# Kernel optimization log

Measured on AMD Instinct MI355X. Metric: run time of the kernel, lower is better.

## Reference

```python
import jax, jax.numpy as jnp
import numpy as np

B, T, C = 8, 1024, 2048
N_HEAD = 16
HEAD = C // N_HEAD  # 128


def setup_inputs() -> dict:
    key = jax.random.key(0)
    k1, k2, k3 = jax.random.split(key, 3)
    scale = 0.02
    x = jax.random.normal(k1, (B, T, C), dtype=jnp.float32)
    W_attn = jax.random.normal(k2, (C, 3 * C), dtype=jnp.float32) * scale
    b_attn = jnp.zeros((3 * C,), dtype=jnp.float32)
    W_proj = jax.random.normal(k3, (C, C), dtype=jnp.float32) * scale
    b_proj = jnp.zeros((C,), dtype=jnp.float32)
    return {"x": x, "W_attn": W_attn, "b_attn": b_attn, "W_proj": W_proj, "b_proj": b_proj}


def reference(x, W_attn, b_attn, W_proj, b_proj):
    Bq, Tq, Cq = x.shape
    qkv = x @ W_attn + b_attn                       # [B,T,3C]
    q, k, v = jnp.split(qkv, 3, axis=2)             # each [B,T,C]
    def heads(t):
        return t.reshape(Bq, Tq, N_HEAD, HEAD).transpose(0, 2, 1, 3)  # [B,H,T,D]
    q, k, v = heads(q), heads(k), heads(v)
    scores = jnp.einsum('bhqd,bhkd->bhqk', q, k) / jnp.sqrt(jnp.float32(HEAD))
    causal = jnp.tril(jnp.ones((Tq, Tq), dtype=bool))
    scores = jnp.where(causal, scores, jnp.float32(-1e9))
    attn = jax.nn.softmax(scores, axis=-1)          # [B,H,T,T]
    y = jnp.einsum('bhqk,bhkd->bhqd', attn, v)      # [B,H,T,D]
    y = y.transpose(0, 2, 1, 3).reshape(Bq, Tq, Cq) # [B,T,C]
    return y @ W_proj + b_proj
```

## Files before the change

### kernel.cpp

```cpp
#include <hip/hip_runtime.h>
#include <hip/hip_bf16.h>


typedef unsigned short u16;
typedef unsigned int u32;
typedef __bf16 bf16x8 __attribute__((ext_vector_type(8)));
typedef float f32x4 __attribute__((ext_vector_type(4)));

#define B_ 8
#define T_ 1024
#define C_ 2048
#define NH 16
#define HD 128
#define BH (B_*NH)

__device__ __forceinline__ u16 f2b(float f){
  __bf16 h = (__bf16)f; return __builtin_bit_cast(u16, h);
}
__device__ __forceinline__ unsigned pk2(float x, float y){
  return (unsigned)f2b(x) | ((unsigned)f2b(y) << 16);
}
__device__ __forceinline__ bf16x8 ldfrag(const u16* p){
  uint4 u = *(const uint4*)p; return __builtin_bit_cast(bf16x8, u);
}
__device__ __forceinline__ void glds16(const u16* g, const u16* l){
  __builtin_amdgcn_global_load_lds(
      (const __attribute__((address_space(1))) void*)g,
      (__attribute__((address_space(3))) void*)l, 16, 0, 0);
}
__device__ __forceinline__ void sbar(){
  __builtin_amdgcn_sched_barrier(0);
  __builtin_amdgcn_s_barrier();
  __builtin_amdgcn_sched_barrier(0);
}

__global__ __launch_bounds__(256) void prep(
    const float* __restrict__ W_attn, u16* __restrict__ Wat,
    const float* __restrict__ W_proj, u16* __restrict__ Wpt,
    const float4* __restrict__ x4, ushort4* __restrict__ xb4, int do_cvt)
{
  __shared__ u16 tile[64][65];
  const int t = threadIdx.x;
  const int z = blockIdx.z;
  if (z == 1 && blockIdx.x >= 32){
    if (!do_cvt) return;
    const int n4 = (B_*T_*C_)/4;
    int i = ((blockIdx.x - 32)*32 + blockIdx.y)*256 + t;
    const int stride = 2048*256;
    for (; i < n4; i += stride){
      float4 f = x4[i];
      ushort4 o; o.x = f2b(f.x); o.y = f2b(f.y); o.z = f2b(f.z); o.w = f2b(f.w);
      xb4[i] = o;
    }
    return;
  }
  const float* in = (z == 0) ? W_attn : W_proj;
  u16* outp       = (z == 0) ? Wat    : Wpt;
  const int R = 2048, C = (z == 0) ? 6144 : 2048;
  const int r0 = blockIdx.y * 64, c0 = blockIdx.x * 64;
#pragma unroll
  for (int ii = 0; ii < 16; ++ii){
    int idx = t + ii*256; int r = idx >> 6, c = idx & 63;
    tile[r][c] = f2b(in[(size_t)(r0 + r)*C + c0 + c]);
  }
  __syncthreads();
#pragma unroll
  for (int ii = 0; ii < 16; ++ii){
    int idx = t + ii*256; int r = idx >> 6, c = idx & 63;
    outp[(size_t)(c0 + r)*R + r0 + c] = tile[c][r];
  }
}

__device__ __forceinline__ void qkv_epilogue(
    const f32x4 acc[4][4], const float* bias, int bx, int by,
    int wm, int wn, int lq, int ln,
    u16* qb, u16* kb, u16* vb)
{
  const int tensor = bx >> 4, h = bx & 15, b = by >> 3, t0 = (by & 7)*128;
  u16* tb = tensor==0 ? qb : (tensor==1 ? kb : vb);
  u16* op = tb + ((size_t)(b*NH + h)*T_ + t0)*HD;
#pragma unroll
  for (int j=0;j<4;j++){
    const float bv = bias[bx*128 + wn*64 + j*16 + ln];
    const int n = wn*64 + j*16 + ln;
#pragma unroll
    for (int i=0;i<4;i++){
      const int m0 = wm*64 + i*16 + lq*4;
#pragma unroll
      for (int r=0;r<4;r++)
        op[(size_t)(m0 + r)*HD + n] = f2b(acc[i][j][r] + bv);
    }
  }
}

__global__ __launch_bounds__(512,2) void gemm_qkv_8p(
    const u16* __restrict__ Xb, const u16* __restrict__ Wt,
    const float* __restrict__ bias,
    u16* __restrict__ qb, u16* __restrict__ kb, u16* __restrict__ vb)
{
  __shared__ u16 lds[2][2][256*64];
  const int t = threadIdx.x;
  const int lane = t & 63, wid = t >> 6;
  const int lq = lane >> 4, ln = lane & 15;
  const int wm = wid >> 2, wn = wid & 3;

  const int bid0 = blockIdx.x;
  const int bid = (bid0 & 7)*96 + (bid0 >> 3);
  const int bx = bid % 24, by = bid / 24;

  const int rl  = (wid << 4) + (lane >> 3);
  const int sw0 = (lane & 7) ^ (rl & 7);
  const u16* Ag = Xb + ((size_t)(by*256) + rl)*2048;
  const u16* Bg = Wt + ((size_t)(bx*256) + rl)*2048;
  const size_t q0off = (size_t)sw0*8;
  const size_t q1off = (size_t)8*2048 + (size_t)sw0*8;

#define STAGE(buf_, op_, h_, T_) do { \
    const u16* s_ = (op_ ? Bg : Ag) + (size_t)(h_)*(128*2048) + (size_t)(T_)*64; \
    const u16* d_ = &lds[buf_][op_][(((h_)*128) + (wid<<4))*64]; \
    glds16(s_ + q0off, d_); \
    glds16(s_ + q1off, d_ + 8*64); \
  } while(0)

  const int swr0 = (0*4 + lq) ^ (ln & 7);
  const int swr1 = (1*4 + lq) ^ (ln & 7);

  const f32x4 fz = {0.f,0.f,0.f,0.f};
  f32x4 acc[8][4];
#pragma unroll
  for (int f=0;f<8;f++)
#pragma unroll
    for (int g=0;g<4;g++) acc[f][g] = fz;

  STAGE(0,0,0,0); STAGE(0,0,1,0); STAGE(0,1,0,0); STAGE(0,1,1,0);
  STAGE(1,1,0,1); STAGE(1,1,1,1); STAGE(1,0,0,1);
  asm volatile("s_waitcnt vmcnt(6)" ::: "memory");
  sbar();

  for (int T = 0; T < 32; ++T){
    const int b = T & 1;
    const u16* As = lds[b][0];
    const u16* Bs = lds[b][1];
    bf16x8 a0[4][2], a4[4][2], bfr[4][2];

#pragma unroll
    for (int f=0;f<4;f++){
      a0[f][0]  = ldfrag(&As[(wm*128 + f*16 + ln)*64 + swr0*8]);
      a0[f][1]  = ldfrag(&As[(wm*128 + f*16 + ln)*64 + swr1*8]);
      bfr[f][0] = ldfrag(&Bs[(wn*64  + f*16 + ln)*64 + swr0*8]);
      bfr[f][1] = ldfrag(&Bs[(wn*64  + f*16 + ln)*64 + swr1*8]);
    }
    if (T+1 < 32) STAGE(b^1, 0, 1, T+1);
    sbar();
    __builtin_amdgcn_s_setprio(1);
#pragma unroll
    for (int f=0;f<4;f++)
#pragma unroll
      for (int g=0;g<2;g++){
        acc[f][g] = __builtin_amdgcn_mfma_f32_16x16x32_bf16(a0[f][0], bfr[g][0], acc[f][g], 0,0,0);
        acc[f][g] = __builtin_amdgcn_mfma_f32_16x16x32_bf16(a0[f][1], bfr[g][1], acc[f][g], 0,0,0);
      }
    __builtin_amdgcn_s_setprio(0);
    sbar();

#pragma unroll
    for (int f=0;f<4;f++){
      a4[f][0] = ldfrag(&As[(wm*128 + (f+4)*16 + ln)*64 + swr0*8]);
      a4[f][1] = ldfrag(&As[(wm*128 + (f+4)*16 + ln)*64 + swr1*8]);
    }
    if (T+2 < 32) STAGE(b, 1, 0, T+2);
    sbar();
    __builtin_amdgcn_s_setprio(1);
#pragma unroll
    for (int f=0;f<4;f++)
#pragma unroll
      for (int g=0;g<2;g++){
        acc[f+4][g] = __builtin_amdgcn_mfma_f32_16x16x32_bf16(a4[f][0], bfr[g][0], acc[f+4][g], 0,0,0);
        acc[f+4][g] = __builtin_amdgcn_mfma_f32_16x16x32_bf16(a4[f][1], bfr[g][1], acc[f+4][g], 0,0,0);
      }
    __builtin_amdgcn_s_setprio(0);
    sbar();

    if (T+2 < 32) STAGE(b, 1, 1, T+2);
    sbar();
    __builtin_amdgcn_s_setprio(1);
#pragma unroll
    for (int f=0;f<4;f++)
#pragma unroll
      for (int g=2;g<4;g++){
        acc[f+4][g] = __builtin_amdgcn_mfma_f32_16x16x32_bf16(a4[f][0], bfr[g][0], acc[f+4][g], 0,0,0);
        acc[f+4][g] = __builtin_amdgcn_mfma_f32_16x16x32_bf16(a4[f][1], bfr[g][1], acc[f+4][g], 0,0,0);
      }
    __builtin_amdgcn_s_setprio(0);
    sbar();

    if (T+2 < 32) STAGE(b, 0, 0, T+2);
    if (T >= 30) asm volatile("s_waitcnt vmcnt(0)" ::: "memory");
    else         asm volatile("s_waitcnt vmcnt(6)" ::: "memory");
    sbar();
    __builtin_amdgcn_s_setprio(1);
#pragma unroll
    for (int f=0;f<4;f++)
#pragma unroll
      for (int g=2;g<4;g++){
        acc[f][g] = __builtin_amdgcn_mfma_f32_16x16x32_bf16(a0[f][0], bfr[g][0], acc[f][g], 0,0,0);
        acc[f][g] = __builtin_amdgcn_mfma_f32_16x16x32_bf16(a0[f][1], bfr[g][1], acc[f][g], 0,0,0);
      }
    __builtin_amdgcn_s_setprio(0);
    sbar();
  }
#undef STAGE

  const int tensor = bx >> 3;
  u16* tb = tensor==0 ? qb : (tensor==1 ? kb : vb);
  const int m_base = by*256 + wm*128;
#pragma unroll
  for (int g=0; g<4; ++g){
    const int ncol = (bx & 7)*256 + wn*64 + g*16 + ln;
    const float bv = bias[tensor*2048 + ncol];
    const int h = ncol >> 7, d = ncol & 127;
#pragma unroll
    for (int f=0; f<8; ++f){
      const int m0 = m_base + f*16 + lq*4;
      const int bb = m0 >> 10, tt = m0 & 1023;
      u16* op = tb + ((size_t)(bb*NH + h)*T_ + tt)*HD + d;
#pragma unroll
      for (int r=0;r<4;++r)
        op[(size_t)r*HD] = f2b(acc[f][g][r] + bv);
    }
  }
}

__global__ __launch_bounds__(512,2) void gemm_proj_8p(
    const u16* __restrict__ Y, const u16* __restrict__ Wt,
    const float* __restrict__ bias, float* __restrict__ outp)
{
  __shared__ u16 lds[2][2][256*64];
  const int t = threadIdx.x;
  const int lane = t & 63, wid = t >> 6;
  const int lq = lane >> 4, ln = lane & 15;
  const int wm = wid >> 2, wn = wid & 3;

  const int bid0 = blockIdx.x;
  const int bid = (bid0 & 7)*32 + (bid0 >> 3);
  const int bx = bid & 7, by = bid >> 3;

  const int rl  = (wid << 4) + (lane >> 3);
  const int sw0 = (lane & 7) ^ (rl & 7);
  const u16* Bg = Wt + ((size_t)(bx*256) + rl)*2048;
  const size_t bq0 = (size_t)sw0*8;
  const size_t arow0 = ((size_t)(by >> 2)*16)*1024 + (size_t)(by & 3)*256 + rl;

#define STAGEP(buf_, op_, h_, Tt_) do { \
    const u16* d_ = &lds[buf_][op_][(((h_)*128) + (wid<<4))*64]; \
    if (op_){ \
      const u16* s_ = Bg + (size_t)(h_)*(128*2048) + (size_t)(Tt_)*64; \
      glds16(s_ + bq0, d_); \
      glds16(s_ + (size_t)8*2048 + bq0, d_ + 8*64); \
    } else { \
      const u16* s_ = Y + (arow0 + (size_t)((Tt_) >> 1)*1024 + (size_t)(h_)*128)*128 \
                        + ((Tt_) & 1)*64 + sw0*8; \
      glds16(s_, d_); \
      glds16(s_ + 8*128, d_ + 8*64); \
    } \
  } while(0)

  const int swr0 = (0*4 + lq) ^ (ln & 7);
  const int swr1 = (1*4 + lq) ^ (ln & 7);

  const f32x4 fz = {0.f,0.f,0.f,0.f};
  f32x4 acc[8][4];
#pragma unroll
  for (int f=0;f<8;f++)
#pragma unroll
    for (int g=0;g<4;g++) acc[f][g] = fz;

  STAGEP(0,0,0,0); STAGEP(0,0,1,0); STAGEP(0,1,0,0); STAGEP(0,1,1,0);
  STAGEP(1,1,0,1); STAGEP(1,1,1,1); STAGEP(1,0,0,1);
  asm volatile("s_waitcnt vmcnt(6)" ::: "memory");
  sbar();

  for (int T = 0; T < 32; ++T){
    const int b = T & 1;
    const u16* As = lds[b][0];
    const u16* Bs = lds[b][1];
    bf16x8 a0[4][2], a4[4][2], bfr[4][2];

#pragma unroll
    for (int f=0;f<4;f++){
      a0[f][0]  = ldfrag(&As[(wm*128 + f*16 + ln)*64 + swr0*8]);
      a0[f][1]  = ldfrag(&As[(wm*128 + f*16 + ln)*64 + swr1*8]);
      bfr[f][0] = ldfrag(&Bs[(wn*64  + f*16 + ln)*64 + swr0*8]);
      bfr[f][1] = ldfrag(&Bs[(wn*64  + f*16 + ln)*64 + swr1*8]);
    }
    if (T+1 < 32) STAGEP(b^1, 0, 1, T+1);
    sbar();
    __builtin_amdgcn_s_setprio(1);
#pragma unroll
    for (int f=0;f<4;f++)
#pragma unroll
      for (int g=0;g<2;g++){
        acc[f][g] = __builtin_amdgcn_mfma_f32_16x16x32_bf16(a0[f][0], bfr[g][0], acc[f][g], 0,0,0);
        acc[f][g] = __builtin_amdgcn_mfma_f32_16x16x32_bf16(a0[f][1], bfr[g][1], acc[f][g], 0,0,0);
      }
    __builtin_amdgcn_s_setprio(0);
    sbar();

#pragma unroll
    for (int f=0;f<4;f++){
      a4[f][0] = ldfrag(&As[(wm*128 + (f+4)*16 + ln)*64 + swr0*8]);
      a4[f][1] = ldfrag(&As[(wm*128 + (f+4)*16 + ln)*64 + swr1*8]);
    }
    if (T+2 < 32) STAGEP(b, 1, 0, T+2);
    sbar();
    __builtin_amdgcn_s_setprio(1);
#pragma unroll
    for (int f=0;f<4;f++)
#pragma unroll
      for (int g=0;g<2;g++){
        acc[f+4][g] = __builtin_amdgcn_mfma_f32_16x16x32_bf16(a4[f][0], bfr[g][0], acc[f+4][g], 0,0,0);
        acc[f+4][g] = __builtin_amdgcn_mfma_f32_16x16x32_bf16(a4[f][1], bfr[g][1], acc[f+4][g], 0,0,0);
      }
    __builtin_amdgcn_s_setprio(0);
    sbar();

    if (T+2 < 32) STAGEP(b, 1, 1, T+2);
    sbar();
    __builtin_amdgcn_s_setprio(1);
#pragma unroll
    for (int f=0;f<4;f++)
#pragma unroll
      for (int g=2;g<4;g++){
        acc[f+4][g] = __builtin_amdgcn_mfma_f32_16x16x32_bf16(a4[f][0], bfr[g][0], acc[f+4][g], 0,0,0);
        acc[f+4][g] = __builtin_amdgcn_mfma_f32_16x16x32_bf16(a4[f][1], bfr[g][1], acc[f+4][g], 0,0,0);
      }
    __builtin_amdgcn_s_setprio(0);
    sbar();

    if (T+2 < 32) STAGEP(b, 0, 0, T+2);
    if (T >= 30) asm volatile("s_waitcnt vmcnt(0)" ::: "memory");
    else         asm volatile("s_waitcnt vmcnt(6)" ::: "memory");
    sbar();
    __builtin_amdgcn_s_setprio(1);
#pragma unroll
    for (int f=0;f<4;f++)
#pragma unroll
      for (int g=2;g<4;g++){
        acc[f][g] = __builtin_amdgcn_mfma_f32_16x16x32_bf16(a0[f][0], bfr[g][0], acc[f][g], 0,0,0);
        acc[f][g] = __builtin_amdgcn_mfma_f32_16x16x32_bf16(a0[f][1], bfr[g][1], acc[f][g], 0,0,0);
      }
    __builtin_amdgcn_s_setprio(0);
    sbar();
  }
#undef STAGEP

  const int m_base = by*256 + wm*128;
#pragma unroll
  for (int g=0; g<4; ++g){
    const int ncol = bx*256 + wn*64 + g*16 + ln;
    const float bv = bias[ncol];
#pragma unroll
    for (int f=0; f<8; ++f){
      const int m0 = m_base + f*16 + lq*4;
      float* op = outp + (size_t)m0*2048 + ncol;
#pragma unroll
      for (int r=0;r<4;++r)
        op[(size_t)r*2048] = acc[f][g][r] + bv;
    }
  }
}

__global__ __launch_bounds__(256,2) void gemm_qkv_f32(
    const float* __restrict__ X, const u16* __restrict__ Wt, const float* __restrict__ bias,
    u16* __restrict__ qb, u16* __restrict__ kb, u16* __restrict__ vb)
{
  __shared__ u16 As[128*32];
  __shared__ u16 Bs[128*32];
  const int t = threadIdx.x;
  const int bx = blockIdx.x, by = blockIdx.y;
  const int lane = t & 63, wv = t >> 6;
  const int lq = lane >> 4, ln = lane & 15;
  const int wm = wv >> 1, wn = wv & 1;

  const int ar = t >> 1, ah = t & 1;
  const float* Ap = X + (size_t)(by*128 + ar)*2048 + ah*16;
  u16* AsW = &As[ar*32 + ah*16];

  const int c0 = t, c1 = 256 + t;
  const u16* Bp0 = Wt + (size_t)(bx*128 + (c0 >> 2))*2048 + (c0 & 3)*8;
  const u16* Bp1 = Wt + (size_t)(bx*128 + (c1 >> 2))*2048 + (c1 & 3)*8;
  const u16* BsW0 = &Bs[(wv*64)*8];
  const u16* BsW1 = &Bs[(256 + wv*64)*8];

  const f32x4 fz = {0.f,0.f,0.f,0.f};
  f32x4 acc[4][4];
#pragma unroll
  for (int i=0;i<4;i++)
#pragma unroll
    for (int j=0;j<4;j++) acc[i][j] = fz;

  for (int kt = 0; kt < 64; ++kt){
    float4 a0 = *(const float4*)(Ap);
    float4 a1 = *(const float4*)(Ap + 4);
    float4 a2 = *(const float4*)(Ap + 8);
    float4 a3 = *(const float4*)(Ap + 12);
    Ap += 32;
    __syncthreads();
    uint4 w0, w1;
    w0.x = pk2(a0.x,a0.y); w0.y = pk2(a0.z,a0.w);
    w0.z = pk2(a1.x,a1.y); w0.w = pk2(a1.z,a1.w);
    w1.x = pk2(a2.x,a2.y); w1.y = pk2(a2.z,a2.w);
    w1.z = pk2(a3.x,a3.y); w1.w = pk2(a3.z,a3.w);
    *(uint4*)(AsW) = w0; *(uint4*)(AsW + 8) = w1;
    glds16(Bp0, BsW0);
    glds16(Bp1, BsW1);
    Bp0 += 32; Bp1 += 32;
    __syncthreads();
    bf16x8 af[4], bf[4];
#pragma unroll
    for (int i=0;i<4;i++) af[i] = ldfrag(&As[(wm*64 + i*16 + ln)*32 + lq*8]);
#pragma unroll
    for (int j=0;j<4;j++) bf[j] = ldfrag(&Bs[(wn*64 + j*16 + ln)*32 + lq*8]);
#pragma unroll
    for (int i=0;i<4;i++)
#pragma unroll
      for (int j=0;j<4;j++)
        acc[i][j] = __builtin_amdgcn_mfma_f32_16x16x32_bf16(af[i], bf[j], acc[i][j], 0,0,0);
  }
  qkv_epilogue(acc, bias, bx, by, wm, wn, lq, ln, qb, kb, vb);
}

__global__ __launch_bounds__(256,2) void attn_fwd(
    u16* qy, const u16* __restrict__ kk, const u16* __restrict__ vv)
{
  __shared__ u16 Ks[2][64*128];
  __shared__ u16 Vt[2][128*64];
  const int bh = blockIdx.x, qt = 7 - blockIdx.y;
  const int t = threadIdx.x;
  const int lane = t & 63, wv = t >> 6;
  const int lq = lane >> 4, ln = lane & 15;

  bf16x8 qf[2][4];
#pragma unroll
  for (int i=0;i<2;i++)
#pragma unroll
    for (int kc=0;kc<4;kc++){
      int qrow = qt*128 + wv*32 + i*16 + ln;
      qf[i][kc] = ldfrag(&qy[((size_t)bh*T_ + qrow)*HD + kc*32 + lq*8]);
    }

  const f32x4 fz = {0.f,0.f,0.f,0.f};
  f32x4 o[2][8];
#pragma unroll
  for (int i=0;i<2;i++)
#pragma unroll
    for (int jd=0;jd<8;jd++) o[i][jd] = fz;
  float mi[2] = {-1e30f, -1e30f}, li[2] = {0.f, 0.f};

  const float scale = 0.08838834764831843f;
  const int vp = t & 31, vdh = t >> 5;
  const int nkt = 2*qt + 2;

  uint4 kreg[4];
  uint4 vr[4];
  {
    const uint4* ksrc = (const uint4*)(kk + (size_t)bh*T_*HD);
#pragma unroll
    for (int ii=0; ii<4; ++ii) kreg[ii] = ksrc[t + ii*256];
    const u16* v0 = &vv[((size_t)bh*T_ + 2*vp)*HD + vdh*16];
    vr[0] = *(const uint4*)(v0);
    vr[1] = *(const uint4*)(v0 + 8);
    vr[2] = *(const uint4*)(v0 + HD);
    vr[3] = *(const uint4*)(v0 + HD + 8);
  }

  for (int kt = 0; kt < nkt; ++kt){
    const int b = kt & 1;
    uint4* kdst = (uint4*)Ks[b];
#pragma unroll
    for (int ii=0; ii<4; ++ii){
      const int c = t + ii*256;
      kdst[(c & ~15) | ((c & 15) ^ ((c >> 4) & 7))] = kreg[ii];
    }
#pragma unroll
    for (int half=0; half<2; ++half){
      const u16* e0 = (const u16*)&vr[half];
      const u16* e1 = (const u16*)&vr[2+half];
#pragma unroll
      for (int j=0; j<8; ++j){
        const int d = vdh*16 + half*8 + j;
        const u32 w = (u32)e0[j] | ((u32)e1[j] << 16);
        *(u32*)&Vt[b][d*64 + ((2*vp) ^ (j<<3))] = w;
      }
    }
    {
      const int ktn = (kt+1 < nkt) ? kt+1 : kt;
      const uint4* ksrc = (const uint4*)(kk + ((size_t)bh*T_ + ktn*64)*HD);
#pragma unroll
      for (int ii=0; ii<4; ++ii) kreg[ii] = ksrc[t + ii*256];
      const u16* v0 = &vv[((size_t)bh*T_ + ktn*64 + 2*vp)*HD + vdh*16];
      vr[0] = *(const uint4*)(v0);
      vr[1] = *(const uint4*)(v0 + 8);
      vr[2] = *(const uint4*)(v0 + HD);
      vr[3] = *(const uint4*)(v0 + HD + 8);
    }
    __syncthreads();

    const bool active = (kt*64) <= (qt*128 + wv*32 + 31);
    if (active){

    f32x4 s[2][4];
#pragma unroll
    for (int i=0;i<2;i++)
#pragma unroll
      for (int j=0;j<4;j++) s[i][j] = fz;
    __builtin_amdgcn_s_setprio(1);
#pragma unroll
    for (int j=0;j<4;j++){
      bf16x8 kf[4];
      const int krow = j*16 + ln;
      const int ksw = (krow & 7) << 3;
#pragma unroll
      for (int kc=0;kc<4;kc++)
        kf[kc] = ldfrag(&Ks[b][krow*128 + ((kc*32 + lq*8) ^ ksw)]);
#pragma unroll
      for (int i=0;i<2;i++)
#pragma unroll
        for (int kc=0;kc<4;kc++)
          s[i][j] = __builtin_amdgcn_mfma_f32_16x16x32_bf16(kf[kc], qf[i][kc], s[i][j], 0,0,0);
    }
    __builtin_amdgcn_s_setprio(0);

#pragma unroll
    for (int i=0;i<2;i++){
      const int qg = qt*128 + wv*32 + i*16 + ln;
#pragma unroll
      for (int j=0;j<4;j++)
#pragma unroll
        for (int r=0;r<4;r++){
          const int kg = kt*64 + j*16 + lq*4 + r;
          float sv = s[i][j][r]*scale;
          s[i][j][r] = (kg > qg) ? -1e30f : sv;
        }
    }

    float mx[2];
#pragma unroll
    for (int i=0;i<2;i++){
      float m = s[i][0][0];
#pragma unroll
      for (int j=0;j<4;j++)
#pragma unroll
        for (int r=0;r<4;r++) m = fmaxf(m, s[i][j][r]);
      m = fmaxf(m, __shfl_xor(m, 16));
      m = fmaxf(m, __shfl_xor(m, 32));
      mx[i] = m;
    }
    bool ok = (mx[0] <= mi[0] + 8.0f) && (mx[1] <= mi[1] + 8.0f);
    if (!__all((int)ok)){
#pragma unroll
      for (int i=0;i<2;i++){
        float mnew = fmaxf(mi[i], mx[i]);
        float alpha = __expf(mi[i] - mnew);
        li[i] *= alpha;
        mi[i] = mnew;
#pragma unroll
        for (int jd=0;jd<8;jd++)
#pragma unroll
          for (int r=0;r<4;r++) o[i][jd][r] *= alpha;
      }
    }
#pragma unroll
    for (int i=0;i<2;i++){
      float rs = 0.f;
#pragma unroll
      for (int j=0;j<4;j++)
#pragma unroll
        for (int r=0;r<4;r++){
          float p = __expf(s[i][j][r] - mi[i]);
          s[i][j][r] = p; rs += p;
        }
      rs += __shfl_xor(rs, 16);
      rs += __shfl_xor(rs, 32);
      li[i] += rs;
    }

    bf16x8 pb[2][2];
#pragma unroll
    for (int i=0;i<2;i++)
#pragma unroll
      for (int c=0;c<2;c++){
        uint4 w;
        w.x = pk2(s[i][c][0],   s[i][c][1]);
        w.y = pk2(s[i][c][2],   s[i][c][3]);
        w.z = pk2(s[i][c+2][0], s[i][c+2][1]);
        w.w = pk2(s[i][c+2][2], s[i][c+2][3]);
        pb[i][c] = __builtin_bit_cast(bf16x8, w);
      }
    __builtin_amdgcn_s_setprio(1);
#pragma unroll
    for (int jd=0;jd<8;jd++){
      const int vrow = jd*16 + ln;
      const int vsw = (vrow & 7) << 3;
#pragma unroll
      for (int c=0;c<2;c++){
        uint2 vlo = *(const uint2*)&Vt[b][vrow*64 + ((c*16     + lq*4) ^ vsw)];
        uint2 vhi = *(const uint2*)&Vt[b][vrow*64 + (((c+2)*16 + lq*4) ^ vsw)];
        uint4 vw; vw.x = vlo.x; vw.y = vlo.y; vw.z = vhi.x; vw.w = vhi.y;
        const bf16x8 va = __builtin_bit_cast(bf16x8, vw);
#pragma unroll
        for (int i=0;i<2;i++)
          o[i][jd] = __builtin_amdgcn_mfma_f32_16x16x32_bf16(va, pb[i][c], o[i][jd], 0,0,0);
      }
    }
    __builtin_amdgcn_s_setprio(0);

    }
  }

#pragma unroll
  for (int i=0;i<2;i++){
    const float inv = 1.f / li[i];
    const int q = qt*128 + wv*32 + i*16 + ln;
#pragma unroll
    for (int jd=0;jd<8;jd++){
      ushort4 w;
      w.x = f2b(o[i][jd][0] * inv);
      w.y = f2b(o[i][jd][1] * inv);
      w.z = f2b(o[i][jd][2] * inv);
      w.w = f2b(o[i][jd][3] * inv);
      *(ushort4*)&qy[((size_t)bh*T_ + q)*HD + jd*16 + lq*4] = w;
    }
  }
}

extern "C" void kernel_launch(void* const* d_in, const int* in_sizes, int n_in,
                              void* d_out, int out_size, void* d_ws, size_t ws_size,
                              hipStream_t stream)
{
  const float* x      = (const float*)d_in[0];
  const float* W_attn = (const float*)d_in[1];
  const float* b_attn = (const float*)d_in[2];
  const float* W_proj = (const float*)d_in[3];
  const float* b_proj = (const float*)d_in[4];
  float* out = (float*)d_out;

  u16* Wat = (u16*)d_ws;
  u16* Wpt = Wat + (size_t)6144*2048;
  u16* qb  = Wpt + (size_t)2048*2048;
  u16* xb  = qb  + (size_t)BH*T_*HD;
  u16* kb  = (u16*)d_out;
  u16* vb  = kb + (size_t)BH*T_*HD;

  const size_t need = ((size_t)6144*2048 + (size_t)2048*2048
                       + 2*(size_t)BH*T_*HD) * sizeof(u16);
  const int big_ws = (ws_size >= need) ? 1 : 0;

  hipLaunchKernelGGL(prep, dim3(96,32,2), dim3(256,1,1), 0, stream,
                     W_attn, Wat, W_proj, Wpt,
                     (const float4*)x, (ushort4*)xb, big_ws);
  if (big_ws){
    hipLaunchKernelGGL(gemm_qkv_8p, dim3(768,1,1), dim3(512,1,1), 0, stream,
                       xb, Wat, b_attn, qb, kb, vb);
  } else {
    hipLaunchKernelGGL(gemm_qkv_f32, dim3(48,64,1), dim3(256,1,1), 0, stream,
                       x, Wat, b_attn, qb, kb, vb);
  }
  hipLaunchKernelGGL(attn_fwd, dim3(BH,8,1), dim3(256,1,1), 0, stream,
                     qb, kb, vb);
  hipLaunchKernelGGL(gemm_proj_8p, dim3(256,1,1), dim3(512,1,1), 0, stream,
                     qb, Wpt, b_proj, out);
}
```

Before: 520.3 us.

## Load K fragments directly from global memory and use exp2-based softmax

The attention kernel drops the shared-memory K tile and its register prefetch. Each wave now reads its K MFMA fragments straight from global memory (relying on L1/L2 caching), which removes the LDS writes for K and halves the kernel's LDS footprint, possibly raising occupancy. The softmax is also rescaled into base 2 (scale multiplied by log2(e), threshold adjusted) so exp2f replaces __expf. In exchange, the four waves issue redundant global reads of K and lose the prefetch overlap for it, so K latency is exposed on the MFMA path.

```diff
diff --git a/kernel.cpp b/kernel.cpp
--- a/kernel.cpp
+++ b/kernel.cpp
@@ -433,7 +433,6 @@
 __global__ __launch_bounds__(256,2) void attn_fwd(
     u16* qy, const u16* __restrict__ kk, const u16* __restrict__ vv)
 {
-  __shared__ u16 Ks[2][64*128];
   __shared__ u16 Vt[2][128*64];
   const int bh = blockIdx.x, qt = 7 - blockIdx.y;
   const int t = threadIdx.x;
@@ -457,16 +456,14 @@
     for (int jd=0;jd<8;jd++) o[i][jd] = fz;
   float mi[2] = {-1e30f, -1e30f}, li[2] = {0.f, 0.f};
 
-  const float scale = 0.08838834764831843f;
+  const float SCALE2 = 0.12751744900765176f;
+  const float THR2   = 11.541560327111707f;
   const int vp = t & 31, vdh = t >> 5;
+  const u16* kbase = kk + (size_t)bh*T_*HD;
   const int nkt = 2*qt + 2;
 
-  uint4 kreg[4];
   uint4 vr[4];
   {
-    const uint4* ksrc = (const uint4*)(kk + (size_t)bh*T_*HD);
-#pragma unroll
-    for (int ii=0; ii<4; ++ii) kreg[ii] = ksrc[t + ii*256];
     const u16* v0 = &vv[((size_t)bh*T_ + 2*vp)*HD + vdh*16];
     vr[0] = *(const uint4*)(v0);
     vr[1] = *(const uint4*)(v0 + 8);
@@ -476,12 +473,6 @@
 
   for (int kt = 0; kt < nkt; ++kt){
     const int b = kt & 1;
-    uint4* kdst = (uint4*)Ks[b];
-#pragma unroll
-    for (int ii=0; ii<4; ++ii){
-      const int c = t + ii*256;
-      kdst[(c & ~15) | ((c & 15) ^ ((c >> 4) & 7))] = kreg[ii];
-    }
 #pragma unroll
     for (int half=0; half<2; ++half){
       const u16* e0 = (const u16*)&vr[half];
@@ -495,9 +486,6 @@
     }
     {
       const int ktn = (kt+1 < nkt) ? kt+1 : kt;
-      const uint4* ksrc = (const uint4*)(kk + ((size_t)bh*T_ + ktn*64)*HD);
-#pragma unroll
-      for (int ii=0; ii<4; ++ii) kreg[ii] = ksrc[t + ii*256];
       const u16* v0 = &vv[((size_t)bh*T_ + ktn*64 + 2*vp)*HD + vdh*16];
       vr[0] = *(const uint4*)(v0);
       vr[1] = *(const uint4*)(v0 + 8);
@@ -518,11 +506,10 @@
 #pragma unroll
     for (int j=0;j<4;j++){
       bf16x8 kf[4];
-      const int krow = j*16 + ln;
-      const int ksw = (krow & 7) << 3;
+      const u16* krow = kbase + (size_t)(kt*64 + j*16 + ln)*HD;
 #pragma unroll
       for (int kc=0;kc<4;kc++)
-        kf[kc] = ldfrag(&Ks[b][krow*128 + ((kc*32 + lq*8) ^ ksw)]);
+        kf[kc] = ldfrag(krow + kc*32 + lq*8);
 #pragma unroll
       for (int i=0;i<2;i++)
 #pragma unroll
@@ -539,7 +526,7 @@
 #pragma unroll
         for (int r=0;r<4;r++){
           const int kg = kt*64 + j*16 + lq*4 + r;
-          float sv = s[i][j][r]*scale;
+          float sv = s[i][j][r]*SCALE2;
           s[i][j][r] = (kg > qg) ? -1e30f : sv;
         }
     }
@@ -556,12 +543,12 @@
       m = fmaxf(m, __shfl_xor(m, 32));
       mx[i] = m;
     }
-    bool ok = (mx[0] <= mi[0] + 8.0f) && (mx[1] <= mi[1] + 8.0f);
+    bool ok = (mx[0] <= mi[0] + THR2) && (mx[1] <= mi[1] + THR2);
     if (!__all((int)ok)){
 #pragma unroll
       for (int i=0;i<2;i++){
         float mnew = fmaxf(mi[i], mx[i]);
-        float alpha = __expf(mi[i] - mnew);
+        float alpha = exp2f(mi[i] - mnew);
         li[i] *= alpha;
         mi[i] = mnew;
 #pragma unroll
@@ -577,7 +564,7 @@
       for (int j=0;j<4;j++)
 #pragma unroll
         for (int r=0;r<4;r++){
-          float p = __expf(s[i][j][r] - mi[i]);
+          float p = exp2f(s[i][j][r] - mi[i]);
           s[i][j][r] = p; rs += p;
         }
       rs += __shfl_xor(rs, 16);
```

Measured after the change: 551.8 us. 1.06x slower.
